# Kernel optimization log

Hardware: AMD Instinct MI355X
Metric: run time of the kernel (lower is better)

The kernel has to match this reference:

```python
import jax, jax.numpy as jnp
import numpy as np

N = 50000
E = 800000
IN = 64
HID = 64
C = 32          # n_coefficients
K = 50          # number of RBF kernels in ContinuousFilterConvolution
MU = jnp.linspace(0.0, 5.0, K)  # RBF centers
GAMMA = 10.0    # RBF width
EPS = 1e-5


def silu(v):
    return v * jax.nn.sigmoid(v)


def edge_softmax(logits, dst, n):
    # DGL edge_softmax: normalize over incoming edges of each destination node
    m = jax.ops.segment_max(logits, dst, num_segments=n)
    e = jnp.exp(logits - m[dst])
    s = jax.ops.segment_sum(e, dst, num_segments=n)
    return e / s[dst]


def _lin(k, fi, fo):
    return (jax.random.normal(k, (fi, fo), jnp.float32) / np.sqrt(fi)).astype(jnp.float32)


def setup_inputs() -> dict:
    key = jax.random.key(0)
    ks = jax.random.split(key, 24)
    inp = {
        'h': jax.random.normal(ks[0], (N, IN), jnp.float32),
        'x': jax.random.normal(ks[1], (N, 3), jnp.float32),
        'src': jax.random.randint(ks[2], (E,), 0, N),
        'dst': jax.random.randint(ks[3], (E,), 0, N),
        # ContinuousFilterConvolution: linear on h, RBF-filter net on distance
        'W_cf_in': _lin(ks[4], 2 * IN, HID), 'b_cf_in': jnp.zeros((HID,), jnp.float32),
        'W_cf_f': _lin(ks[5], K, HID), 'b_cf_f': jnp.zeros((HID,), jnp.float32),
        # semantic_attention_mlp: Linear(2*IN, 1, bias=False) + SiLU
        'W_sem': _lin(ks[6], 2 * IN, 1),
        # edge_weight_mlp: Linear(2*IN+HID, C) + Tanh
        'W_ew': _lin(ks[7], 2 * IN + HID, C), 'b_ew': jnp.zeros((C,), jnp.float32),
        # post_norm_nlp: Linear(C, HID) + SiLU + Linear(HID, HID)
        'W_pn1': _lin(ks[8], C, HID), 'b_pn1': jnp.zeros((HID,), jnp.float32),
        'W_pn2': _lin(ks[9], HID, HID), 'b_pn2': jnp.zeros((HID,), jnp.float32),
        # node_mlp: Linear(IN+2*HID, HID) + SiLU + Linear(HID, HID)
        'W_n1': _lin(ks[10], IN + 2 * HID, HID), 'b_n1': jnp.zeros((HID,), jnp.float32),
        'W_n2': _lin(ks[11], HID, HID), 'b_n2': jnp.zeros((HID,), jnp.float32),
        # coordinate_mlp: Linear(HID, HID) + SiLU + Linear(HID, 1)
        'W_c1': _lin(ks[12], HID, HID), 'b_c1': jnp.zeros((HID,), jnp.float32),
        'W_c2': _lin(ks[13], HID, 1), 'b_c2': jnp.zeros((1,), jnp.float32),
    }
    return inp


def reference(h, x, src, dst,
              W_cf_in, b_cf_in, W_cf_f, b_cf_f, W_sem,
              W_ew, b_ew, W_pn1, b_pn1, W_pn2, b_pn2,
              W_n1, b_n1, W_n2, b_n2, W_c1, b_c1, W_c2, b_c2):
    n = h.shape[0]
    x_mx = x[src] - x[dst]                                               # [E,3]
    d = jnp.sqrt(jax.nn.relu(jnp.sum(x_mx ** 2, -1, keepdims=True)) + EPS)  # [E,1]
    h_cat = jnp.concatenate([h[src], h[dst]], -1)                        # [E,2*IN]

    # ContinuousFilterConvolution(h_cat, d) -> h_e [E,HID]
    rbf = jnp.exp(-GAMMA * (d - MU) ** 2)                                # [E,K]
    h_e = (h_cat @ W_cf_in + b_cf_in) * silu(rbf @ W_cf_f + b_cf_f)

    # dual edge-softmax attention, combined multiplicatively, re-normalized
    eu = edge_softmax(-d, dst, n)                                        # [E,1]
    sem = edge_softmax(silu(h_cat @ W_sem), dst, n)                      # [E,1]
    tot = edge_softmax(eu * sem, dst, n)                                 # [E,1]

    how = jnp.tanh(jnp.concatenate([h_cat, h_e], -1) @ W_ew + b_ew)      # [E,C]
    h_e_att = tot * h_e                                                  # [E,HID]

    x_att = how[..., None] * (x_mx / (d ** 2))[:, None, :]               # [E,C,3]
    x_att_sum = jax.ops.segment_sum(x_att, dst, num_segments=n)          # [N,C,3]
    nrm = jnp.sqrt(jax.nn.relu(jnp.sum(x_att_sum ** 2, -1)) + EPS)       # [N,C]
    emb = silu(nrm @ W_pn1 + b_pn1) @ W_pn2 + b_pn2                      # [N,HID]

    h_agg = jax.ops.segment_sum(h_e_att, dst, num_segments=n)            # [N,HID]
    h_new = silu(jnp.concatenate([h, h_agg, emb], -1) @ W_n1 + b_n1) @ W_n2 + b_n2

    coef = silu(h_e @ W_c1 + b_c1) @ W_c2 + b_c2                         # [E,1]
    x_new = x + jax.ops.segment_sum(x_mx * coef, dst, num_segments=n)    # [N,3]
    return h_new, x_new
```

## Files before the change

kernel.cpp:

```cpp
#include <hip/hip_runtime.h>
#include <hip/hip_bf16.h>

#define N_NODES 50000
#define N_EDGES 800000
#define SCAN_B 196
#define MAX_DEG 512

typedef short s16x8 __attribute__((ext_vector_type(8)));
typedef float f32x4 __attribute__((ext_vector_type(4)));

__device__ __forceinline__ float silu_f(float v) {
  return v / (1.0f + __expf(-v));
}
__device__ __forceinline__ float tanh_f(float v) {
  return 1.0f - 2.0f / (__expf(2.0f * v) + 1.0f);
}
__device__ __forceinline__ unsigned short f2bf(float f) {
  union { __hip_bfloat16 b; unsigned short u; } cv;
  cv.b = __float2bfloat16(f);
  return cv.u;
}
__device__ __forceinline__ float bf2f(short s) {
  union { unsigned u; float f; } a; a.u = ((unsigned)(unsigned short)s) << 16;
  return a.f;
}

__global__ void hist_kernel(const int* __restrict__ dst, int* __restrict__ deg) {
  int i = blockIdx.x * 256 + threadIdx.x;
  if (i < N_EDGES) atomicAdd(&deg[dst[i]], 1);
}

__global__ __launch_bounds__(256) void scanA_kernel(const int* __restrict__ deg,
                                                    int* __restrict__ bsum) {
  int i = blockIdx.x * 256 + threadIdx.x;
  int lane = threadIdx.x & 63, w = threadIdx.x >> 6;
  int v = (i < N_NODES) ? deg[i] : 0;
  #pragma unroll
  for (int o = 32; o > 0; o >>= 1) v += __shfl_xor(v, o, 64);
  __shared__ int ws_[4];
  if (lane == 0) ws_[w] = v;
  __syncthreads();
  if (threadIdx.x == 0) bsum[blockIdx.x] = ws_[0] + ws_[1] + ws_[2] + ws_[3];
}

__global__ void scanB_kernel(const int* __restrict__ bsum, int* __restrict__ bpre) {
  int lane = threadIdx.x;
  int carry = 0;
  for (int base = 0; base < SCAN_B; base += 64) {
    int i = base + lane;
    int v = (i < SCAN_B) ? bsum[i] : 0;
    int sv = v;
    #pragma unroll
    for (int o = 1; o < 64; o <<= 1) {
      int u = __shfl_up(sv, o, 64);
      if (lane >= o) sv += u;
    }
    if (i < SCAN_B) bpre[i] = carry + sv - v;
    carry += __shfl(sv, 63, 64);
  }
}

__global__ __launch_bounds__(256) void scanC_kernel(const int* __restrict__ deg,
                                                    const int* __restrict__ bpre,
                                                    int* __restrict__ off) {
  int i = blockIdx.x * 256 + threadIdx.x;
  int lane = threadIdx.x & 63, w = threadIdx.x >> 6;
  int v = (i < N_NODES) ? deg[i] : 0;
  int sv = v;
  #pragma unroll
  for (int o = 1; o < 64; o <<= 1) {
    int u = __shfl_up(sv, o, 64);
    if (lane >= o) sv += u;
  }
  __shared__ int ws_[4], wp_[4];
  if (lane == 63) ws_[w] = sv;
  __syncthreads();
  if (threadIdx.x == 0) {
    int s = 0;
    #pragma unroll
    for (int j = 0; j < 4; ++j) { wp_[j] = s; s += ws_[j]; }
  }
  __syncthreads();
  if (i < N_NODES) off[i + 1] = bpre[blockIdx.x] + wp_[w] + sv;
  if (i == 0) off[0] = 0;
}

__global__ void scatter_kernel(const int* __restrict__ dst, const int* __restrict__ off,
                               int* __restrict__ cur, int* __restrict__ eperm) {
  int i = blockIdx.x * 256 + threadIdx.x;
  if (i < N_EDGES) {
    int dn = dst[i];
    int pos = atomicAdd(&cur[dn], 1);
    eperm[off[dn] + pos] = i;
  }
}

__global__ void prep_kernel(const float* __restrict__ Wcfin, const float* __restrict__ Wcff,
                            const float* __restrict__ Wew, const float* __restrict__ Wsem,
                            const float* __restrict__ Wc1,
                            const float* __restrict__ Wpn1, const float* __restrict__ Wpn2,
                            const float* __restrict__ Wn1, const float* __restrict__ Wn2,
                            const float* __restrict__ h,
                            short* __restrict__ WpreT, short* __restrict__ WcffT,
                            short* __restrict__ WewBT, short* __restrict__ Wc1T,
                            short* __restrict__ Wpn1T, short* __restrict__ Wpn2T,
                            short* __restrict__ Wn1T, short* __restrict__ Wn2T,
                            short* __restrict__ h_bf) {
  int t = blockIdx.x * 256 + threadIdx.x;
  int stride = gridDim.x * 256;
  for (int i = t; i < 224 * 64; i += stride) {
    int n = i >> 6, k = i & 63;
    int half = (n >= 112) ? 1 : 0;
    int c = n - half * 112;
    float v = 0.f;
    if (c < 64)       v = Wcfin[(half * 64 + k) * 64 + c];
    else if (c < 96)  v = Wew[(half * 64 + k) * 32 + (c - 64)];
    else if (c == 96) v = Wsem[half * 64 + k];
    WpreT[i] = (short)f2bf(v);
  }
  for (int i = t; i < 64 * 64; i += stride) {
    int n = i >> 6, k = i & 63;
    WcffT[i] = (k < 50) ? (short)f2bf(Wcff[k * 64 + n]) : (short)0;
  }
  for (int i = t; i < 32 * 64; i += stride) {
    int n = i >> 6, k = i & 63;
    WewBT[i] = (short)f2bf(Wew[(128 + k) * 32 + n]);
  }
  for (int i = t; i < 64 * 64; i += stride) {
    int n = i >> 6, k = i & 63;
    Wc1T[i] = (short)f2bf(Wc1[k * 64 + n]);
  }
  for (int i = t; i < 64 * 32; i += stride) {
    int n = i >> 5, k = i & 31;
    Wpn1T[i] = (short)f2bf(Wpn1[k * 64 + n]);
  }
  for (int i = t; i < 64 * 64; i += stride) {
    int n = i >> 6, k = i & 63;
    Wpn2T[i] = (short)f2bf(Wpn2[k * 64 + n]);
  }
  for (int i = t; i < 64 * 192; i += stride) {
    int n = i / 192, k = i - n * 192;
    Wn1T[i] = (short)f2bf(Wn1[k * 64 + n]);
  }
  for (int i = t; i < 64 * 64; i += stride) {
    int n = i >> 6, k = i & 63;
    Wn2T[i] = (short)f2bf(Wn2[k * 64 + n]);
  }
  for (int i = t; i < (N_NODES * 64) / 4; i += stride) {
    float4 v = reinterpret_cast<const float4*>(h)[i];
    ushort4 u;
    u.x = f2bf(v.x); u.y = f2bf(v.y); u.z = f2bf(v.z); u.w = f2bf(v.w);
    reinterpret_cast<ushort4*>(h_bf)[i] = u;
  }
}

__global__ __launch_bounds__(256) void pre_node_kernel(
    const short* __restrict__ h_bf, const short* __restrict__ WpreT,
    short* __restrict__ preS, short* __restrict__ preD)
{
  __shared__ short hs[64][72];
  const int t = threadIdx.x;
  const int w = t >> 6, lane = t & 63;
  const int n0 = blockIdx.x * 64;
  const int rbase = w * 16;

  #pragma unroll
  for (int u = 0; u < 2; ++u) {
    int c = lane + u * 64;
    int riw = c >> 3, col8 = (c & 7) * 8;
    int node = n0 + rbase + riw; if (node >= N_NODES) node = N_NODES - 1;
    *reinterpret_cast<s16x8*>(&hs[rbase + riw][col8]) =
        *reinterpret_cast<const s16x8*>(&h_bf[(size_t)node * 64 + col8]);
  }

  const int lr = lane & 15, lg = lane >> 4;
  const int arow = rbase + lr;
  const int k8 = lg * 8;
  const f32x4 z = {0.f, 0.f, 0.f, 0.f};

  #pragma unroll
  for (int half = 0; half < 2; ++half) {
    short* out = half ? preD : preS;
    #pragma unroll
    for (int j = 0; j < 7; ++j) {
      f32x4 acc = z;
      #pragma unroll
      for (int kb = 0; kb < 64; kb += 32) {
        s16x8 a = *reinterpret_cast<const s16x8*>(&hs[arow][kb + k8]);
        s16x8 b = *reinterpret_cast<const s16x8*>(&WpreT[(half * 112 + j * 16 + lr) * 64 + kb + k8]);
        acc = __builtin_amdgcn_mfma_f32_16x16x32_bf16(a, b, acc, 0, 0, 0);
      }
      #pragma unroll
      for (int r = 0; r < 4; ++r) {
        int node = n0 + rbase + lg * 4 + r;
        if (node < N_NODES) out[(size_t)node * 112 + j * 16 + lr] = (short)f2bf(acc[r]);
      }
    }
  }
}

__global__ __launch_bounds__(256, 6) void edge_kernel(
    const float* __restrict__ x,
    const int* __restrict__ src, const int* __restrict__ dst,
    const int* __restrict__ eperm,
    const short* __restrict__ preS, const short* __restrict__ preD,
    const float* __restrict__ b_cf_in,
    const short* __restrict__ WcffT, const float* __restrict__ b_cf_f,
    const short* __restrict__ WewBT, const float* __restrict__ b_ew,
    const short* __restrict__ Wc1T, const float* __restrict__ b_c1,
    const float* __restrict__ W_c2, const float* __restrict__ b_c2,
    float* __restrict__ d_arr, float* __restrict__ xmx_arr,
    float2* __restrict__ e12_arr, float* __restrict__ coef_arr,
    short* __restrict__ he_g, short* __restrict__ how_g)
{
  __shared__ short hlin[64][72];
  __shared__ short rbf_s[64][72];
  __shared__ short ewsum[64][40];

  const int t = threadIdx.x;
  const int p0 = blockIdx.x * 64;
  const int le = t >> 2, q = t & 3;
  const int p_edge = p0 + le;

  const int e = eperm[p_edge];
  const int sn = src[e], dn = dst[e];

  float mx0 = x[sn * 3 + 0] - x[dn * 3 + 0];
  float mx1 = x[sn * 3 + 1] - x[dn * 3 + 1];
  float mx2 = x[sn * 3 + 2] - x[dn * 3 + 2];
  float d = sqrtf(mx0 * mx0 + mx1 * mx1 + mx2 * mx2 + 1e-5f);
  if (q == 0) {
    d_arr[p_edge] = d;
    xmx_arr[p_edge * 3 + 0] = mx0;
    xmx_arr[p_edge * 3 + 1] = mx1;
    xmx_arr[p_edge * 3 + 2] = mx2;
  }

  {
    const short* ps = preS + (size_t)sn * 112;
    const short* pd = preD + (size_t)dn * 112;
    #pragma unroll
    for (int ci = 0; ci < 3; ++ci) {
      int c = q * 3 + ci;
      s16x8 a = *reinterpret_cast<const s16x8*>(ps + c * 8);
      s16x8 b = *reinterpret_cast<const s16x8*>(pd + c * 8);
      s16x8 r;
      #pragma unroll
      for (int u = 0; u < 8; ++u) r[u] = (short)f2bf(bf2f(a[u]) + bf2f(b[u]));
      short* dstp = (c < 8) ? &hlin[le][c * 8] : &ewsum[le][(c - 8) * 8];
      *reinterpret_cast<s16x8*>(dstp) = r;
    }
    if (q == 3) {
      float sem = bf2f(ps[96]) + bf2f(pd[96]);
      float2 ee;
      ee.x = __expf(-d);
      ee.y = __expf(silu_f(sem));
      e12_arr[p_edge] = ee;
    }
  }

  {
    int kb = q * 16;
    s16x8 lo, hi;
    #pragma unroll 16
    for (int u = 0; u < 16; ++u) {
      int k = kb + u;
      float mu = (float)k * (5.0f / 49.0f);
      float dd = d - mu;
      float val = (k < 50) ? __expf(-10.0f * dd * dd) : 0.0f;
      short sv = (short)f2bf(val);
      if (u < 8) lo[u] = sv; else hi[u - 8] = sv;
    }
    *reinterpret_cast<s16x8*>(&rbf_s[le][kb]) = lo;
    *reinterpret_cast<s16x8*>(&rbf_s[le][kb + 8]) = hi;
  }

  const int w = t >> 6, lane = t & 63;
  const int lr = lane & 15, lg = lane >> 4;
  const int arow = w * 16 + lr;
  const int k8 = lg * 8;
  const f32x4 z = {0.f, 0.f, 0.f, 0.f};

  f32x4 fac[4] = {z, z, z, z};
  #pragma unroll
  for (int kb = 0; kb < 64; kb += 32) {
    s16x8 a = *reinterpret_cast<const s16x8*>(&rbf_s[arow][kb + k8]);
    #pragma unroll
    for (int j = 0; j < 4; ++j) {
      s16x8 b = *reinterpret_cast<const s16x8*>(&WcffT[(j * 16 + lr) * 64 + kb + k8]);
      fac[j] = __builtin_amdgcn_mfma_f32_16x16x32_bf16(a, b, fac[j], 0, 0, 0);
    }
  }

  #pragma unroll
  for (int j = 0; j < 4; ++j) {
    int col = j * 16 + lr;
    float bi = b_cf_in[col], bf_ = b_cf_f[col];
    #pragma unroll
    for (int r = 0; r < 4; ++r) {
      int row = w * 16 + lg * 4 + r;
      float lin = bf2f(hlin[row][col]);
      float he = (lin + bi) * silu_f(fac[j][r] + bf_);
      hlin[row][col] = (short)f2bf(he);
    }
  }

  #pragma unroll
  for (int u = 0; u < 2; ++u) {
    int chunk = lane + u * 64;
    int riw = chunk >> 3, col8 = (chunk & 7) * 8;
    s16x8 v = *reinterpret_cast<const s16x8*>(&hlin[w * 16 + riw][col8]);
    *reinterpret_cast<s16x8*>(&he_g[((size_t)(p0 + w * 16 + riw)) * 64 + col8]) = v;
  }

  {
    f32x4 ew[2];
    #pragma unroll
    for (int j = 0; j < 2; ++j) {
      #pragma unroll
      for (int r = 0; r < 4; ++r)
        ew[j][r] = bf2f(ewsum[w * 16 + lg * 4 + r][j * 16 + lr]);
    }
    #pragma unroll
    for (int kb = 0; kb < 64; kb += 32) {
      s16x8 a = *reinterpret_cast<const s16x8*>(&hlin[arow][kb + k8]);
      #pragma unroll
      for (int j = 0; j < 2; ++j) {
        s16x8 b = *reinterpret_cast<const s16x8*>(&WewBT[(j * 16 + lr) * 64 + kb + k8]);
        ew[j] = __builtin_amdgcn_mfma_f32_16x16x32_bf16(a, b, ew[j], 0, 0, 0);
      }
    }
    #pragma unroll
    for (int j = 0; j < 2; ++j) {
      int col = j * 16 + lr;
      float be = b_ew[col];
      #pragma unroll
      for (int r = 0; r < 4; ++r)
        ewsum[w * 16 + lg * 4 + r][col] = (short)f2bf(tanh_f(ew[j][r] + be));
    }
  }

  {
    f32x4 c[4] = {z, z, z, z};
    #pragma unroll
    for (int kb = 0; kb < 64; kb += 32) {
      s16x8 a = *reinterpret_cast<const s16x8*>(&hlin[arow][kb + k8]);
      #pragma unroll
      for (int j = 0; j < 4; ++j) {
        s16x8 b = *reinterpret_cast<const s16x8*>(&Wc1T[(j * 16 + lr) * 64 + kb + k8]);
        c[j] = __builtin_amdgcn_mfma_f32_16x16x32_bf16(a, b, c[j], 0, 0, 0);
      }
    }
    float p[4] = {0.f, 0.f, 0.f, 0.f};
    #pragma unroll
    for (int j = 0; j < 4; ++j) {
      int col = j * 16 + lr;
      float bc = b_c1[col], wc = W_c2[col];
      #pragma unroll
      for (int r = 0; r < 4; ++r) p[r] += silu_f(c[j][r] + bc) * wc;
    }
    #pragma unroll
    for (int r = 0; r < 4; ++r) {
      p[r] += __shfl_xor(p[r], 1, 64);
      p[r] += __shfl_xor(p[r], 2, 64);
      p[r] += __shfl_xor(p[r], 4, 64);
      p[r] += __shfl_xor(p[r], 8, 64);
    }
    if (lr == 0) {
      float bc2 = b_c2[0];
      #pragma unroll
      for (int r = 0; r < 4; ++r)
        coef_arr[p0 + w * 16 + lg * 4 + r] = p[r] + bc2;
    }
  }

  {
    int riw = lane >> 2, col8 = (lane & 3) * 8;
    s16x8 v = *reinterpret_cast<const s16x8*>(&ewsum[w * 16 + riw][col8]);
    *reinterpret_cast<s16x8*>(&how_g[((size_t)(p0 + w * 16 + riw)) * 32 + col8]) = v;
  }
}

__global__ __launch_bounds__(256) void node_agg_kernel(
    const int* __restrict__ off, const float* __restrict__ d_arr,
    const float2* __restrict__ e12_arr, const short* __restrict__ he_g,
    const float* __restrict__ coef_arr, const float* __restrict__ xmx_arr,
    const short* __restrict__ how_g, const float* __restrict__ x,
    float* __restrict__ tot_un,
    short* __restrict__ hagg_bf, short* __restrict__ nrm_bf,
    float* __restrict__ x_out)
{
  __shared__ float tot_s[4][MAX_DEG];
  int w = threadIdx.x >> 6, lane = threadIdx.x & 63;
  int n = blockIdx.x * 4 + w;
  if (n >= N_NODES) return;
  int b = off[n], e = off[n + 1];
  const bool fits = (e - b) <= MAX_DEG;

  float s1 = 0.f, s2 = 0.f;
  for (int p = b + lane; p < e; p += 64) {
    float2 ee = e12_arr[p];
    s1 += ee.x; s2 += ee.y;
    float pr = ee.x * ee.y;
    if (fits) tot_s[w][p - b] = pr; else tot_un[p] = pr;
  }
  #pragma unroll
  for (int o = 32; o > 0; o >>= 1) { s1 += __shfl_xor(s1, o, 64); s2 += __shfl_xor(s2, o, 64); }
  float r12 = (1.f / s1) * (1.f / s2);

  float s3 = 0.f;
  for (int p = b + lane; p < e; p += 64) {
    float pr = fits ? tot_s[w][p - b] : tot_un[p];
    float ex = __expf(pr * r12);
    s3 += ex;
    if (fits) tot_s[w][p - b] = ex; else tot_un[p] = ex;
  }
  #pragma unroll
  for (int o = 32; o > 0; o >>= 1) s3 += __shfl_xor(s3, o, 64);
  float inv3 = 1.f / s3;
  __threadfence_block();

  float acc = 0.f;
  float xv = (lane < 3) ? x[n * 3 + lane] : 0.f;
  for (int p = b; p < e; ++p) {
    float tot = (fits ? tot_s[w][p - b] : tot_un[p]) * inv3;
    acc += tot * bf2f(he_g[(size_t)p * 64 + lane]);
    if (lane < 3) xv += xmx_arr[p * 3 + lane] * coef_arr[p];
  }
  hagg_bf[(size_t)n * 64 + lane] = (short)f2bf(acc);
  if (lane < 3) x_out[n * 3 + lane] = xv;

  int c = lane & 31, par = lane >> 5;
  float a0 = 0.f, a1 = 0.f, a2 = 0.f;
  for (int p = b + par; p < e; p += 2) {
    float wv = bf2f(how_g[(size_t)p * 32 + c]);
    float dd = d_arr[p];
    float s = wv / (dd * dd);
    a0 += s * xmx_arr[p * 3 + 0];
    a1 += s * xmx_arr[p * 3 + 1];
    a2 += s * xmx_arr[p * 3 + 2];
  }
  a0 += __shfl_xor(a0, 32, 64);
  a1 += __shfl_xor(a1, 32, 64);
  a2 += __shfl_xor(a2, 32, 64);
  if (lane < 32)
    nrm_bf[(size_t)n * 32 + c] =
        (short)f2bf(sqrtf(fmaxf(a0 * a0 + a1 * a1 + a2 * a2, 0.f) + 1e-5f));
}

__global__ __launch_bounds__(256) void node_mlp_kernel(
    const short* __restrict__ h_bf, const short* __restrict__ hagg_bf,
    const short* __restrict__ nrm_bf,
    const short* __restrict__ Wpn1T, const float* __restrict__ b_pn1,
    const short* __restrict__ Wpn2T, const float* __restrict__ b_pn2,
    const short* __restrict__ Wn1T, const float* __restrict__ b_n1,
    const short* __restrict__ Wn2T, const float* __restrict__ b_n2,
    float* __restrict__ h_out)
{
  __shared__ short cat[64][200];
  __shared__ short tbuf[64][72];

  const int t = threadIdx.x;
  const int w = t >> 6, lane = t & 63;
  const int n0 = blockIdx.x * 64;
  const int rbase = w * 16;

  #pragma unroll
  for (int u = 0; u < 2; ++u) {
    int c = lane + u * 64;
    int riw = c >> 3, col8 = (c & 7) * 8;
    int node = n0 + rbase + riw; if (node >= N_NODES) node = N_NODES - 1;
    *reinterpret_cast<s16x8*>(&cat[rbase + riw][col8]) =
        *reinterpret_cast<const s16x8*>(&h_bf[(size_t)node * 64 + col8]);
    *reinterpret_cast<s16x8*>(&cat[rbase + riw][64 + col8]) =
        *reinterpret_cast<const s16x8*>(&hagg_bf[(size_t)node * 64 + col8]);
  }
  {
    int riw = lane >> 2, col8 = (lane & 3) * 8;
    int node = n0 + rbase + riw; if (node >= N_NODES) node = N_NODES - 1;
    *reinterpret_cast<s16x8*>(&tbuf[rbase + riw][col8]) =
        *reinterpret_cast<const s16x8*>(&nrm_bf[(size_t)node * 32 + col8]);
  }

  const int lr = lane & 15, lg = lane >> 4;
  const int arow = rbase + lr;
  const int k8 = lg * 8;
  const f32x4 z = {0.f, 0.f, 0.f, 0.f};

  {
    f32x4 c1[4] = {z, z, z, z};
    s16x8 a = *reinterpret_cast<const s16x8*>(&tbuf[arow][k8]);
    #pragma unroll
    for (int j = 0; j < 4; ++j) {
      s16x8 b = *reinterpret_cast<const s16x8*>(&Wpn1T[(j * 16 + lr) * 32 + k8]);
      c1[j] = __builtin_amdgcn_mfma_f32_16x16x32_bf16(a, b, c1[j], 0, 0, 0);
    }
    #pragma unroll
    for (int j = 0; j < 4; ++j) {
      int col = j * 16 + lr; float bb = b_pn1[col];
      #pragma unroll
      for (int r = 0; r < 4; ++r)
        tbuf[rbase + lg * 4 + r][col] = (short)f2bf(silu_f(c1[j][r] + bb));
    }
  }
  {
    f32x4 c2[4] = {z, z, z, z};
    #pragma unroll
    for (int kb = 0; kb < 64; kb += 32) {
      s16x8 a = *reinterpret_cast<const s16x8*>(&tbuf[arow][kb + k8]);
      #pragma unroll
      for (int j = 0; j < 4; ++j) {
        s16x8 b = *reinterpret_cast<const s16x8*>(&Wpn2T[(j * 16 + lr) * 64 + kb + k8]);
        c2[j] = __builtin_amdgcn_mfma_f32_16x16x32_bf16(a, b, c2[j], 0, 0, 0);
      }
    }
    #pragma unroll
    for (int j = 0; j < 4; ++j) {
      int col = j * 16 + lr; float bb = b_pn2[col];
      #pragma unroll
      for (int r = 0; r < 4; ++r)
        cat[rbase + lg * 4 + r][128 + col] = (short)f2bf(c2[j][r] + bb);
    }
  }
  {
    f32x4 c3[4] = {z, z, z, z};
    #pragma unroll
    for (int kb = 0; kb < 192; kb += 32) {
      s16x8 a = *reinterpret_cast<const s16x8*>(&cat[arow][kb + k8]);
      #pragma unroll
      for (int j = 0; j < 4; ++j) {
        s16x8 b = *reinterpret_cast<const s16x8*>(&Wn1T[(j * 16 + lr) * 192 + kb + k8]);
        c3[j] = __builtin_amdgcn_mfma_f32_16x16x32_bf16(a, b, c3[j], 0, 0, 0);
      }
    }
    #pragma unroll
    for (int j = 0; j < 4; ++j) {
      int col = j * 16 + lr; float bb = b_n1[col];
      #pragma unroll
      for (int r = 0; r < 4; ++r)
        tbuf[rbase + lg * 4 + r][col] = (short)f2bf(silu_f(c3[j][r] + bb));
    }
  }
  {
    f32x4 c4[4] = {z, z, z, z};
    #pragma unroll
    for (int kb = 0; kb < 64; kb += 32) {
      s16x8 a = *reinterpret_cast<const s16x8*>(&tbuf[arow][kb + k8]);
      #pragma unroll
      for (int j = 0; j < 4; ++j) {
        s16x8 b = *reinterpret_cast<const s16x8*>(&Wn2T[(j * 16 + lr) * 64 + kb + k8]);
        c4[j] = __builtin_amdgcn_mfma_f32_16x16x32_bf16(a, b, c4[j], 0, 0, 0);
      }
    }
    #pragma unroll
    for (int j = 0; j < 4; ++j) {
      int col = j * 16 + lr; float bb = b_n2[col];
      #pragma unroll
      for (int r = 0; r < 4; ++r) {
        int node = n0 + rbase + lg * 4 + r;
        if (node < N_NODES) h_out[(size_t)node * 64 + col] = c4[j][r] + bb;
      }
    }
  }
}

extern "C" void kernel_launch(void* const* d_in, const int* in_sizes, int n_in,
                              void* d_out, int out_size, void* d_ws, size_t ws_size,
                              hipStream_t stream) {
  const float* h      = (const float*)d_in[0];
  const float* x      = (const float*)d_in[1];
  const int*   src    = (const int*)d_in[2];
  const int*   dst    = (const int*)d_in[3];
  const float* W_cf_in = (const float*)d_in[4];
  const float* b_cf_in = (const float*)d_in[5];
  const float* W_cf_f  = (const float*)d_in[6];
  const float* b_cf_f  = (const float*)d_in[7];
  const float* W_sem   = (const float*)d_in[8];
  const float* W_ew    = (const float*)d_in[9];
  const float* b_ew    = (const float*)d_in[10];
  const float* W_pn1   = (const float*)d_in[11];
  const float* b_pn1   = (const float*)d_in[12];
  const float* W_pn2   = (const float*)d_in[13];
  const float* b_pn2   = (const float*)d_in[14];
  const float* W_n1    = (const float*)d_in[15];
  const float* b_n1    = (const float*)d_in[16];
  const float* W_n2    = (const float*)d_in[17];
  const float* b_n2    = (const float*)d_in[18];
  const float* W_c1    = (const float*)d_in[19];
  const float* b_c1    = (const float*)d_in[20];
  const float* W_c2    = (const float*)d_in[21];
  const float* b_c2    = (const float*)d_in[22];

  char* ws = (char*)d_ws;
  size_t o = 0;
  auto take = [&](size_t bytes) {
    void* p = ws + o;
    o = (o + bytes + 255) & ~(size_t)255;
    return p;
  };
  int* deg    = (int*)take((size_t)N_NODES * 4);
  int* off    = (int*)take((size_t)(N_NODES + 1) * 4);
  int* cur    = (int*)take((size_t)N_NODES * 4);
  int* eperm  = (int*)take((size_t)N_EDGES * 4);
  int* bsum   = (int*)take((size_t)SCAN_B * 4);
  int* bpre   = (int*)take((size_t)SCAN_B * 4);
  float* d_arr = (float*)take((size_t)N_EDGES * 4);
  float* xmx   = (float*)take((size_t)N_EDGES * 12);
  float2* e12  = (float2*)take((size_t)N_EDGES * 8);
  float* coef  = (float*)take((size_t)N_EDGES * 4);
  float* tot_un = (float*)take((size_t)N_EDGES * 4);
  short* he   = (short*)take((size_t)N_EDGES * 64 * 2);
  short* how  = (short*)take((size_t)N_EDGES * 32 * 2);
  short* hagg_bf = (short*)take((size_t)N_NODES * 64 * 2);
  short* nrm_bf  = (short*)take((size_t)N_NODES * 32 * 2);
  short* WpreT  = (short*)take((size_t)224 * 64 * 2);
  short* WcffT  = (short*)take((size_t)64 * 64 * 2);
  short* WewBT  = (short*)take((size_t)32 * 64 * 2);
  short* Wc1T   = (short*)take((size_t)64 * 64 * 2);
  short* Wpn1T  = (short*)take((size_t)64 * 32 * 2);
  short* Wpn2T  = (short*)take((size_t)64 * 64 * 2);
  short* Wn1T   = (short*)take((size_t)64 * 192 * 2);
  short* Wn2T   = (short*)take((size_t)64 * 64 * 2);
  short* h_bf   = (short*)take((size_t)N_NODES * 64 * 2);
  short* preS   = (short*)take((size_t)N_NODES * 112 * 2);
  short* preD   = (short*)take((size_t)N_NODES * 112 * 2);

  float* h_out = (float*)d_out;
  float* x_out = h_out + (size_t)N_NODES * 64;

  hipMemsetAsync(deg, 0, (size_t)N_NODES * 4, stream);
  hipMemsetAsync(cur, 0, (size_t)N_NODES * 4, stream);

  hist_kernel<<<N_EDGES / 256, 256, 0, stream>>>(dst, deg);
  scanA_kernel<<<SCAN_B, 256, 0, stream>>>(deg, bsum);
  scanB_kernel<<<1, 64, 0, stream>>>(bsum, bpre);
  scanC_kernel<<<SCAN_B, 256, 0, stream>>>(deg, bpre, off);
  scatter_kernel<<<N_EDGES / 256, 256, 0, stream>>>(dst, off, cur, eperm);
  prep_kernel<<<128, 256, 0, stream>>>(W_cf_in, W_cf_f, W_ew, W_sem, W_c1,
                                       W_pn1, W_pn2, W_n1, W_n2, h,
                                       WpreT, WcffT, WewBT, Wc1T,
                                       Wpn1T, Wpn2T, Wn1T, Wn2T, h_bf);
  pre_node_kernel<<<(N_NODES + 63) / 64, 256, 0, stream>>>(h_bf, WpreT, preS, preD);

  edge_kernel<<<N_EDGES / 64, 256, 0, stream>>>(
      x, src, dst, eperm, preS, preD,
      b_cf_in, WcffT, b_cf_f,
      WewBT, b_ew, Wc1T, b_c1, W_c2, b_c2,
      d_arr, xmx, e12, coef, he, how);

  node_agg_kernel<<<N_NODES / 4, 256, 0, stream>>>(
      off, d_arr, e12, he, coef, xmx, how, x, tot_un, hagg_bf, nrm_bf, x_out);

  node_mlp_kernel<<<(N_NODES + 63) / 64, 256, 0, stream>>>(
      h_bf, hagg_bf, nrm_bf,
      Wpn1T, b_pn1, Wpn2T, b_pn2,
      Wn1T, b_n1, Wn2T, b_n2,
      h_out);
}
```

Measured before the change: 490.9 us.

## Fuse edge aggregation into edge kernel via atomics, precompute attention in separate pass

```diff
diff --git a/kernel.cpp b/kernel.cpp
--- a/kernel.cpp
+++ b/kernel.cpp
@@ -23,6 +23,9 @@
 __device__ __forceinline__ float bf2f(short s) {
   union { unsigned u; float f; } a; a.u = ((unsigned)(unsigned short)s) << 16;
   return a.f;
+}
+__device__ __forceinline__ void atomAdd(float* p, float v) {
+  __hip_atomic_fetch_add(p, v, __ATOMIC_RELAXED, __HIP_MEMORY_SCOPE_AGENT);
 }
 
 __global__ void hist_kernel(const int* __restrict__ dst, int* __restrict__ deg) {
@@ -156,7 +159,8 @@
 
 __global__ __launch_bounds__(256) void pre_node_kernel(
     const short* __restrict__ h_bf, const short* __restrict__ WpreT,
-    short* __restrict__ preS, short* __restrict__ preD)
+    short* __restrict__ preS, short* __restrict__ preD,
+    float* __restrict__ semS, float* __restrict__ semD)
 {
   __shared__ short hs[64][72];
   const int t = threadIdx.x;
@@ -181,6 +185,7 @@
   #pragma unroll
   for (int half = 0; half < 2; ++half) {
     short* out = half ? preD : preS;
+    float* osem = half ? semD : semS;
     #pragma unroll
     for (int j = 0; j < 7; ++j) {
       f32x4 acc = z;
@@ -193,29 +198,81 @@
       #pragma unroll
       for (int r = 0; r < 4; ++r) {
         int node = n0 + rbase + lg * 4 + r;
-        if (node < N_NODES) out[(size_t)node * 112 + j * 16 + lr] = (short)f2bf(acc[r]);
-      }
-    }
-  }
+        if (node < N_NODES) {
+          if (j < 6) out[(size_t)node * 96 + j * 16 + lr] = (short)f2bf(acc[r]);
+          else if (lr == 0) osem[node] = acc[r];
+        }
+      }
+    }
+  }
+}
+
+__global__ __launch_bounds__(256) void tot_kernel(
+    const int* __restrict__ off, const int* __restrict__ eperm,
+    const int* __restrict__ src, const float* __restrict__ x,
+    const float* __restrict__ semS, const float* __restrict__ semD,
+    float* __restrict__ tot_un, float* __restrict__ tot_arr)
+{
+  __shared__ float tot_s[4][MAX_DEG];
+  int w = threadIdx.x >> 6, lane = threadIdx.x & 63;
+  int n = blockIdx.x * 4 + w;
+  if (n >= N_NODES) return;
+  int b = off[n], e = off[n + 1];
+  const bool fits = (e - b) <= MAX_DEG;
+  float xn0 = x[n * 3 + 0], xn1 = x[n * 3 + 1], xn2 = x[n * 3 + 2];
+  float sdn = semD[n];
+
+  float s1 = 0.f, s2 = 0.f;
+  for (int p = b + lane; p < e; p += 64) {
+    int sn = src[eperm[p]];
+    float m0 = x[sn * 3 + 0] - xn0;
+    float m1 = x[sn * 3 + 1] - xn1;
+    float m2 = x[sn * 3 + 2] - xn2;
+    float d = sqrtf(m0 * m0 + m1 * m1 + m2 * m2 + 1e-5f);
+    float e1 = __expf(-d);
+    float e2 = __expf(silu_f(semS[sn] + sdn));
+    s1 += e1; s2 += e2;
+    float pr = e1 * e2;
+    if (fits) tot_s[w][p - b] = pr; else tot_un[p] = pr;
+  }
+  #pragma unroll
+  for (int o = 32; o > 0; o >>= 1) { s1 += __shfl_xor(s1, o, 64); s2 += __shfl_xor(s2, o, 64); }
+  float r12 = (1.f / s1) * (1.f / s2);
+
+  float s3 = 0.f;
+  for (int p = b + lane; p < e; p += 64) {
+    float pr = fits ? tot_s[w][p - b] : tot_un[p];
+    float ex = __expf(pr * r12);
+    s3 += ex;
+    if (fits) tot_s[w][p - b] = ex; else tot_un[p] = ex;
+  }
+  #pragma unroll
+  for (int o = 32; o > 0; o >>= 1) s3 += __shfl_xor(s3, o, 64);
+  float inv3 = 1.f / s3;
+
+  for (int p = b + lane; p < e; p += 64)
+    tot_arr[p] = (fits ? tot_s[w][p - b] : tot_un[p]) * inv3;
 }
 
 __global__ __launch_bounds__(256, 6) void edge_kernel(
     const float* __restrict__ x,
     const int* __restrict__ src, const int* __restrict__ dst,
-    const int* __restrict__ eperm,
+    const int* __restrict__ eperm, const float* __restrict__ tot_arr,
     const short* __restrict__ preS, const short* __restrict__ preD,
     const float* __restrict__ b_cf_in,
     const short* __restrict__ WcffT, const float* __restrict__ b_cf_f,
     const short* __restrict__ WewBT, const float* __restrict__ b_ew,
     const short* __restrict__ Wc1T, const float* __restrict__ b_c1,
     const float* __restrict__ W_c2, const float* __restrict__ b_c2,
-    float* __restrict__ d_arr, float* __restrict__ xmx_arr,
-    float2* __restrict__ e12_arr, float* __restrict__ coef_arr,
-    short* __restrict__ he_g, short* __restrict__ how_g)
+    float* __restrict__ hagg, float* __restrict__ xatt,
+    float* __restrict__ x_out)
 {
   __shared__ short hlin[64][72];
   __shared__ short rbf_s[64][72];
   __shared__ short ewsum[64][40];
+  __shared__ float coef_s[64];
+  __shared__ float s_mx0[64], s_mx1[64], s_mx2[64], s_id2[64], s_tot[64];
+  __shared__ int s_dn[64];
 
   const int t = threadIdx.x;
   const int p0 = blockIdx.x * 64;
@@ -228,17 +285,18 @@
   float mx0 = x[sn * 3 + 0] - x[dn * 3 + 0];
   float mx1 = x[sn * 3 + 1] - x[dn * 3 + 1];
   float mx2 = x[sn * 3 + 2] - x[dn * 3 + 2];
-  float d = sqrtf(mx0 * mx0 + mx1 * mx1 + mx2 * mx2 + 1e-5f);
+  float d2 = mx0 * mx0 + mx1 * mx1 + mx2 * mx2 + 1e-5f;
+  float d = sqrtf(d2);
   if (q == 0) {
-    d_arr[p_edge] = d;
-    xmx_arr[p_edge * 3 + 0] = mx0;
-    xmx_arr[p_edge * 3 + 1] = mx1;
-    xmx_arr[p_edge * 3 + 2] = mx2;
-  }
-
-  {
-    const short* ps = preS + (size_t)sn * 112;
-    const short* pd = preD + (size_t)dn * 112;
+    s_mx0[le] = mx0; s_mx1[le] = mx1; s_mx2[le] = mx2;
+    s_id2[le] = 1.0f / d2;
+    s_dn[le] = dn;
+    s_tot[le] = tot_arr[p_edge];
+  }
+
+  {
+    const short* ps = preS + (size_t)sn * 96;
+    const short* pd = preD + (size_t)dn * 96;
     #pragma unroll
     for (int ci = 0; ci < 3; ++ci) {
       int c = q * 3 + ci;
@@ -249,13 +307,6 @@
       for (int u = 0; u < 8; ++u) r[u] = (short)f2bf(bf2f(a[u]) + bf2f(b[u]));
       short* dstp = (c < 8) ? &hlin[le][c * 8] : &ewsum[le][(c - 8) * 8];
       *reinterpret_cast<s16x8*>(dstp) = r;
-    }
-    if (q == 3) {
-      float sem = bf2f(ps[96]) + bf2f(pd[96]);
-      float2 ee;
-      ee.x = __expf(-d);
-      ee.y = __expf(silu_f(sem));
-      e12_arr[p_edge] = ee;
     }
   }
 
@@ -305,14 +356,6 @@
     }
   }
 
-  #pragma unroll
-  for (int u = 0; u < 2; ++u) {
-    int chunk = lane + u * 64;
-    int riw = chunk >> 3, col8 = (chunk & 7) * 8;
-    s16x8 v = *reinterpret_cast<const s16x8*>(&hlin[w * 16 + riw][col8]);
-    *reinterpret_cast<s16x8*>(&he_g[((size_t)(p0 + w * 16 + riw)) * 64 + col8]) = v;
-  }
-
   {
     f32x4 ew[2];
     #pragma unroll
@@ -370,87 +413,49 @@
       float bc2 = b_c2[0];
       #pragma unroll
       for (int r = 0; r < 4; ++r)
-        coef_arr[p0 + w * 16 + lg * 4 + r] = p[r] + bc2;
-    }
-  }
-
-  {
-    int riw = lane >> 2, col8 = (lane & 3) * 8;
-    s16x8 v = *reinterpret_cast<const s16x8*>(&ewsum[w * 16 + riw][col8]);
-    *reinterpret_cast<s16x8*>(&how_g[((size_t)(p0 + w * 16 + riw)) * 32 + col8]) = v;
-  }
-}
-
-__global__ __launch_bounds__(256) void node_agg_kernel(
-    const int* __restrict__ off, const float* __restrict__ d_arr,
-    const float2* __restrict__ e12_arr, const short* __restrict__ he_g,
-    const float* __restrict__ coef_arr, const float* __restrict__ xmx_arr,
-    const short* __restrict__ how_g, const float* __restrict__ x,
-    float* __restrict__ tot_un,
-    short* __restrict__ hagg_bf, short* __restrict__ nrm_bf,
-    float* __restrict__ x_out)
-{
-  __shared__ float tot_s[4][MAX_DEG];
-  int w = threadIdx.x >> 6, lane = threadIdx.x & 63;
-  int n = blockIdx.x * 4 + w;
-  if (n >= N_NODES) return;
-  int b = off[n], e = off[n + 1];
-  const bool fits = (e - b) <= MAX_DEG;
-
-  float s1 = 0.f, s2 = 0.f;
-  for (int p = b + lane; p < e; p += 64) {
-    float2 ee = e12_arr[p];
-    s1 += ee.x; s2 += ee.y;
-    float pr = ee.x * ee.y;
-    if (fits) tot_s[w][p - b] = pr; else tot_un[p] = pr;
-  }
-  #pragma unroll
-  for (int o = 32; o > 0; o >>= 1) { s1 += __shfl_xor(s1, o, 64); s2 += __shfl_xor(s2, o, 64); }
-  float r12 = (1.f / s1) * (1.f / s2);
-
-  float s3 = 0.f;
-  for (int p = b + lane; p < e; p += 64) {
-    float pr = fits ? tot_s[w][p - b] : tot_un[p];
-    float ex = __expf(pr * r12);
-    s3 += ex;
-    if (fits) tot_s[w][p - b] = ex; else tot_un[p] = ex;
-  }
-  #pragma unroll
-  for (int o = 32; o > 0; o >>= 1) s3 += __shfl_xor(s3, o, 64);
-  float inv3 = 1.f / s3;
-  __threadfence_block();
-
-  float acc = 0.f;
-  float xv = (lane < 3) ? x[n * 3 + lane] : 0.f;
-  for (int p = b; p < e; ++p) {
-    float tot = (fits ? tot_s[w][p - b] : tot_un[p]) * inv3;
-    acc += tot * bf2f(he_g[(size_t)p * 64 + lane]);
-    if (lane < 3) xv += xmx_arr[p * 3 + lane] * coef_arr[p];
-  }
-  hagg_bf[(size_t)n * 64 + lane] = (short)f2bf(acc);
-  if (lane < 3) x_out[n * 3 + lane] = xv;
-
-  int c = lane & 31, par = lane >> 5;
-  float a0 = 0.f, a1 = 0.f, a2 = 0.f;
-  for (int p = b + par; p < e; p += 2) {
-    float wv = bf2f(how_g[(size_t)p * 32 + c]);
-    float dd = d_arr[p];
-    float s = wv / (dd * dd);
-    a0 += s * xmx_arr[p * 3 + 0];
-    a1 += s * xmx_arr[p * 3 + 1];
-    a2 += s * xmx_arr[p * 3 + 2];
-  }
-  a0 += __shfl_xor(a0, 32, 64);
-  a1 += __shfl_xor(a1, 32, 64);
-  a2 += __shfl_xor(a2, 32, 64);
-  if (lane < 32)
-    nrm_bf[(size_t)n * 32 + c] =
-        (short)f2bf(sqrtf(fmaxf(a0 * a0 + a1 * a1 + a2 * a2, 0.f) + 1e-5f));
+        coef_s[w * 16 + lg * 4 + r] = p[r] + bc2;
+    }
+  }
+
+  {
+    const int c31 = lane & 31;
+    const bool hi = lane >= 32;
+    float acc_h = 0.f, acc_a = 0.f, acc_b = 0.f, acc_x = 0.f;
+    int nid_prev = s_dn[w * 16];
+    #pragma unroll
+    for (int r = 0; r < 16; ++r) {
+      int row = w * 16 + r;
+      int nid = s_dn[row];
+      if (nid != nid_prev) {
+        atomAdd(&hagg[(size_t)nid_prev * 64 + lane], acc_h);
+        atomAdd(&xatt[(size_t)nid_prev * 96 + (hi ? 32 : 0) + c31], acc_a);
+        if (!hi) atomAdd(&xatt[(size_t)nid_prev * 96 + 64 + lane], acc_b);
+        if (lane < 3) atomAdd(&x_out[nid_prev * 3 + lane], acc_x);
+        acc_h = acc_a = acc_b = acc_x = 0.f;
+        nid_prev = nid;
+      }
+      float tot = s_tot[row];
+      acc_h += tot * bf2f(hlin[row][lane]);
+      float id2 = s_id2[row];
+      float m0 = s_mx0[row], m1 = s_mx1[row], m2 = s_mx2[row];
+      float hw = bf2f(ewsum[row][c31]) * id2;
+      acc_a += hw * (hi ? m1 : m0);
+      if (!hi) acc_b += hw * m2;
+      if (lane < 3) {
+        float cf = coef_s[row];
+        acc_x += cf * (lane == 0 ? m0 : (lane == 1 ? m1 : m2));
+      }
+    }
+    atomAdd(&hagg[(size_t)nid_prev * 64 + lane], acc_h);
+    atomAdd(&xatt[(size_t)nid_prev * 96 + (hi ? 32 : 0) + c31], acc_a);
+    if (!hi) atomAdd(&xatt[(size_t)nid_prev * 96 + 64 + lane], acc_b);
+    if (lane < 3) atomAdd(&x_out[nid_prev * 3 + lane], acc_x);
+  }
 }
 
 __global__ __launch_bounds__(256) void node_mlp_kernel(
-    const short* __restrict__ h_bf, const short* __restrict__ hagg_bf,
-    const short* __restrict__ nrm_bf,
+    const short* __restrict__ h_bf, const float* __restrict__ hagg,
+    const float* __restrict__ xatt,
     const short* __restrict__ Wpn1T, const float* __restrict__ b_pn1,
     const short* __restrict__ Wpn2T, const float* __restrict__ b_pn2,
     const short* __restrict__ Wn1T, const float* __restrict__ b_n1,
@@ -472,14 +477,26 @@
     int node = n0 + rbase + riw; if (node >= N_NODES) node = N_NODES - 1;
     *reinterpret_cast<s16x8*>(&cat[rbase + riw][col8]) =
         *reinterpret_cast<const s16x8*>(&h_bf[(size_t)node * 64 + col8]);
-    *reinterpret_cast<s16x8*>(&cat[rbase + riw][64 + col8]) =
-        *reinterpret_cast<const s16x8*>(&hagg_bf[(size_t)node * 64 + col8]);
+    float4 v0 = *reinterpret_cast<const float4*>(&hagg[(size_t)node * 64 + col8]);
+    float4 v1 = *reinterpret_cast<const float4*>(&hagg[(size_t)node * 64 + col8 + 4]);
+    s16x8 pk;
+    pk[0] = (short)f2bf(v0.x); pk[1] = (short)f2bf(v0.y);
+    pk[2] = (short)f2bf(v0.z); pk[3] = (short)f2bf(v0.w);
+    pk[4] = (short)f2bf(v1.x); pk[5] = (short)f2bf(v1.y);
+    pk[6] = (short)f2bf(v1.z); pk[7] = (short)f2bf(v1.w);
+    *reinterpret_cast<s16x8*>(&cat[rbase + riw][64 + col8]) = pk;
   }
   {
     int riw = lane >> 2, col8 = (lane & 3) * 8;
     int node = n0 + rbase + riw; if (node >= N_NODES) node = N_NODES - 1;
-    *reinterpret_cast<s16x8*>(&tbuf[rbase + riw][col8]) =
-        *reinterpret_cast<const s16x8*>(&nrm_bf[(size_t)node * 32 + col8]);
+    const float* xa = xatt + (size_t)node * 96;
+    #pragma unroll
+    for (int cc = 0; cc < 8; ++cc) {
+      int c = col8 + cc;
+      float a0 = xa[c], a1 = xa[32 + c], a2 = xa[64 + c];
+      float nr = sqrtf(fmaxf(a0 * a0 + a1 * a1 + a2 * a2, 0.f) + 1e-5f);
+      tbuf[rbase + riw][c] = (short)f2bf(nr);
+    }
   }
 
   const int lr = lane & 15, lg = lane >> 4;
@@ -604,15 +621,12 @@
   int* eperm  = (int*)take((size_t)N_EDGES * 4);
   int* bsum   = (int*)take((size_t)SCAN_B * 4);
   int* bpre   = (int*)take((size_t)SCAN_B * 4);
-  float* d_arr = (float*)take((size_t)N_EDGES * 4);
-  float* xmx   = (float*)take((size_t)N_EDGES * 12);
-  float2* e12  = (float2*)take((size_t)N_EDGES * 8);
-  float* coef  = (float*)take((size_t)N_EDGES * 4);
-  float* tot_un = (float*)take((size_t)N_EDGES * 4);
-  short* he   = (short*)take((size_t)N_EDGES * 64 * 2);
-  short* how  = (short*)take((size_t)N_EDGES * 32 * 2);
-  short* hagg_bf = (short*)take((size_t)N_NODES * 64 * 2);
-  short* nrm_bf  = (short*)take((size_t)N_NODES * 32 * 2);
+  float* tot_un  = (float*)take((size_t)N_EDGES * 4);
+  float* tot_arr = (float*)take((size_t)N_EDGES * 4);
+  float* hagg = (float*)take((size_t)N_NODES * 64 * 4);
+  float* xatt = (float*)take((size_t)N_NODES * 96 * 4);
+  float* semS = (float*)take((size_t)N_NODES * 4);
+  float* semD = (float*)take((size_t)N_NODES * 4);
   short* WpreT  = (short*)take((size_t)224 * 64 * 2);
   short* WcffT  = (short*)take((size_t)64 * 64 * 2);
   short* WewBT  = (short*)take((size_t)32 * 64 * 2);
@@ -622,14 +636,17 @@
   short* Wn1T   = (short*)take((size_t)64 * 192 * 2);
   short* Wn2T   = (short*)take((size_t)64 * 64 * 2);
   short* h_bf   = (short*)take((size_t)N_NODES * 64 * 2);
-  short* preS   = (short*)take((size_t)N_NODES * 112 * 2);
-  short* preD   = (short*)take((size_t)N_NODES * 112 * 2);
+  short* preS   = (short*)take((size_t)N_NODES * 96 * 2);
+  short* preD   = (short*)take((size_t)N_NODES * 96 * 2);
 
   float* h_out = (float*)d_out;
   float* x_out = h_out + (size_t)N_NODES * 64;
 
   hipMemsetAsync(deg, 0, (size_t)N_NODES * 4, stream);
   hipMemsetAsync(cur, 0, (size_t)N_NODES * 4, stream);
+  hipMemsetAsync(hagg, 0, (size_t)N_NODES * 64 * 4, stream);
+  hipMemsetAsync(xatt, 0, (size_t)N_NODES * 96 * 4, stream);
+  hipMemcpyAsync(x_out, x, (size_t)N_NODES * 3 * 4, hipMemcpyDeviceToDevice, stream);
 
   hist_kernel<<<N_EDGES / 256, 256, 0, stream>>>(dst, deg);
   scanA_kernel<<<SCAN_B, 256, 0, stream>>>(deg, bsum);
@@ -640,19 +657,19 @@
                                        W_pn1, W_pn2, W_n1, W_n2, h,
                                        WpreT, WcffT, WewBT, Wc1T,
                                        Wpn1T, Wpn2T, Wn1T, Wn2T, h_bf);
-  pre_node_kernel<<<(N_NODES + 63) / 64, 256, 0, stream>>>(h_bf, WpreT, preS, preD);
+  pre_node_kernel<<<(N_NODES + 63) / 64, 256, 0, stream>>>(h_bf, WpreT, preS, preD,
+                                                           semS, semD);
+  tot_kernel<<<N_NODES / 4, 256, 0, stream>>>(off, eperm, src, x, semS, semD,
+                                              tot_un, tot_arr);
 
   edge_kernel<<<N_EDGES / 64, 256, 0, stream>>>(
-      x, src, dst, eperm, preS, preD,
+      x, src, dst, eperm, tot_arr, preS, preD,
       b_cf_in, WcffT, b_cf_f,
       WewBT, b_ew, Wc1T, b_c1, W_c2, b_c2,
-      d_arr, xmx, e12, coef, he, how);
-
-  node_agg_kernel<<<N_NODES / 4, 256, 0, stream>>>(
-      off, d_arr, e12, he, coef, xmx, how, x, tot_un, hagg_bf, nrm_bf, x_out);
+      hagg, xatt, x_out);
 
   node_mlp_kernel<<<(N_NODES + 63) / 64, 256, 0, stream>>>(
-      h_bf, hagg_bf, nrm_bf,
+      h_bf, hagg, xatt,
       Wpn1T, b_pn1, Wpn2T, b_pn2,
       Wn1T, b_n1, Wn2T, b_n2,
       h_out);
```

Result: faster. 428.9 us (-12.6%).
